# Kernel optimization log

Hardware: AMD Instinct MI355X
Metric: run time of the kernel (lower is better)

The kernel has to match this reference:

```python
import jax, jax.numpy as jnp
import numpy as np


def setup_inputs() -> dict:
    key = jax.random.key(0)
    ks = jax.random.split(key, 6)
    B, C, V, L = 64, 32, 512, 13
    C_OUT = 64
    C_CAT = (2 * 3 + 1) * C  # order*support_len + 1 = 7 blocks -> 224
    x = jax.random.normal(ks[0], (B, C, V, L), dtype=jnp.float32)
    support0 = jax.random.uniform(ks[1], (V, V), dtype=jnp.float32)
    support1 = jax.random.uniform(ks[2], (V, V), dtype=jnp.float32)
    support2 = jax.random.uniform(ks[3], (V, V), dtype=jnp.float32)
    W = jax.random.normal(ks[4], (C_OUT, C_CAT), dtype=jnp.float32) * 0.05
    b = jnp.zeros((C_OUT,), dtype=jnp.float32)
    return {"x": x, "support0": support0, "support1": support1,
            "support2": support2, "W": W, "b": b}


def reference(x, support0, support1, support2, W, b):
    # Graph WaveNet GCN, eval mode (dropout is identity at inference).
    # x: [B, C, V, L]; each support a: [V, V].
    outs = [x]
    for a in (support0, support1, support2):
        x1 = jnp.einsum('ncvl,vw->ncwl', x, a)   # order 1 propagation
        outs.append(x1)
        x2 = jnp.einsum('ncvl,vw->ncwl', x1, a)  # order 2 propagation
        outs.append(x2)
    h = jnp.concatenate(outs, axis=1)            # [B, 7*C, V, L]
    # 1x1 Conv2d == per-(v,l) linear over channels
    h = jnp.einsum('ncvl,oc->novl', h, W) + b[None, :, None, None]
    return h
```

## Files before the change

### kernel.cpp

```cpp
#include <hip/hip_runtime.h>


typedef unsigned short u16;
typedef unsigned int   u32;
typedef __bf16 bf16x8 __attribute__((ext_vector_type(8)));
typedef float  f32x4  __attribute__((ext_vector_type(4)));

#define DEVI static __device__ __forceinline__

#define NB   64
#define NC   32
#define NV   512
#define NL   13
#define CO   64
#define CCAT 224
#define SZA   262144L
#define MSZ   (26624L * 512L)

DEVI u16 f2bf(float f) {
  union { float f; u32 u; } v; v.f = f;
  u32 u = v.u;
  return (u16)((u + 0x7fffu + ((u >> 16) & 1u)) >> 16);
}

DEVI void gl2lds16(const void* g, void* l) {
  __builtin_amdgcn_global_load_lds((__attribute__((address_space(1))) void*)g,
                                   (__attribute__((address_space(3))) void*)l, 16, 0, 0);
}

__global__ __launch_bounds__(256) void prep_A(const float* __restrict__ A0,
                                              const float* __restrict__ A1,
                                              const float* __restrict__ A2,
                                              u16* __restrict__ BT,
                                              u16* __restrict__ ABF) {
  const int s = blockIdx.z;
  const float* A = (s == 0) ? A0 : ((s == 1) ? A1 : A2);
  u16* abf = ABF + (long)s * SZA;
  u16* bt  = BT + (long)(2 * s) * SZA;
  __shared__ float t[32][33];
  const int v0 = blockIdx.x * 32, w0 = blockIdx.y * 32;
  const int tid = threadIdx.x;
  for (int i = tid; i < 1024; i += 256) {
    const int r = i >> 5, c = i & 31;
    const float val = A[(long)(v0 + r) * 512 + w0 + c];
    t[r][c] = val;
    abf[(long)(v0 + r) * 512 + w0 + c] = f2bf(val);
  }
  __syncthreads();
  for (int i = tid; i < 1024; i += 256) {
    const int r = i >> 5, c = i & 31;
    bt[(long)(w0 + r) * 512 + v0 + c] = f2bf(t[c][r]);
  }
}

__global__ __launch_bounds__(256) void prep_W(const float* __restrict__ W,
                                              u16* __restrict__ WBF) {
  const int i = blockIdx.x * 256 + threadIdx.x;
  WBF[i] = f2bf(W[i]);
}

__global__ __launch_bounds__(256) void transpose_x(const float* __restrict__ x,
                                                   u16* __restrict__ XT) {
  __shared__ __align__(16) float tile[NV * NL];
  const int bc = blockIdx.x;
  const float4* src4 = (const float4*)(x + (long)bc * (NV * NL));
  float4* t4 = (float4*)tile;
  for (int i = threadIdx.x; i < (NV * NL) / 4; i += 256) t4[i] = src4[i];
  __syncthreads();
  u16* dst = XT + (long)bc * (NL * NV);
  for (int j = threadIdx.x; j < NL * 256; j += 256) {
    const int l = j >> 8, v = (j & 255) * 2;
    const u32 lo = f2bf(tile[v * NL + l]);
    const u32 hi = f2bf(tile[(v + 1) * NL + l]);
    *(u32*)&dst[l * 512 + v] = lo | (hi << 16);
  }
}

__global__ __launch_bounds__(256) void gemm512(const u16* __restrict__ Ag,
                                               const u16* __restrict__ Bg,
                                               u16* __restrict__ Cg,
                                               long aZ, long bZ, long cZ) {
  __shared__ u16 As[128 * 32];
  __shared__ u16 Bs[128 * 32];
  const int p = blockIdx.z;
  const u16* A = Ag + (long)p * aZ;
  const u16* B = Bg + (long)p * bZ;
  u16*       C = Cg + (long)p * cZ;
  const int m0 = blockIdx.y * 128, n0 = blockIdx.x * 128;
  const int tid = threadIdx.x;
  const int lane = tid & 63, wid = tid >> 6;
  const int wm = wid >> 1, wn = wid & 1;
  const int lr = lane & 15, lq = lane >> 4;
  const int srow = lane >> 2, skq = lane & 3;

  f32x4 acc[4][4] = {};

  for (int kt = 0; kt < 16; ++kt) {
    const int k0 = kt * 32;
    __syncthreads();
#pragma unroll
    for (int j = 0; j < 2; ++j) {
      const int rb = wid * 32 + j * 16;
      gl2lds16(A + (long)(m0 + rb + srow) * 512 + (k0 + skq * 8), &As[rb * 32]);
      gl2lds16(B + (long)(n0 + rb + srow) * 512 + (k0 + skq * 8), &Bs[rb * 32]);
    }
    __syncthreads();
    bf16x8 af[4], bv[4];
#pragma unroll
    for (int t = 0; t < 4; ++t) {
      af[t] = *(const bf16x8*)&As[(wm * 64 + t * 16 + lr) * 32 + lq * 8];
      bv[t] = *(const bf16x8*)&Bs[(wn * 64 + t * 16 + lr) * 32 + lq * 8];
    }
#pragma unroll
    for (int i = 0; i < 4; ++i)
#pragma unroll
      for (int j = 0; j < 4; ++j)
        acc[i][j] = __builtin_amdgcn_mfma_f32_16x16x32_bf16(af[i], bv[j], acc[i][j], 0, 0, 0);
  }
#pragma unroll
  for (int i = 0; i < 4; ++i) {
    const int mr = m0 + wm * 64 + i * 16 + lq * 4;
#pragma unroll
    for (int j = 0; j < 4; ++j) {
      const int nc = n0 + wn * 64 + j * 16 + lr;
#pragma unroll
      for (int r = 0; r < 4; ++r)
        C[(long)(mr + r) * 512 + nc] = f2bf(acc[i][j][r]);
    }
  }
}

__global__ __launch_bounds__(256) void gemm_big(const u16* __restrict__ A,
                                                const u16* __restrict__ Bg,
                                                u16* __restrict__ Cg) {
  __shared__ u16 As[128 * 32];
  __shared__ u16 Bs[128 * 32];
  const int p = blockIdx.x >> 2;
  const int n0 = (blockIdx.x & 3) * 128;
  const int m0 = blockIdx.y * 128;
  const u16* B = Bg + (long)p * SZA;
  u16*       C = Cg + (long)p * MSZ;
  const int tid = threadIdx.x;
  const int lane = tid & 63, wid = tid >> 6;
  const int wm = wid >> 1, wn = wid & 1;
  const int lr = lane & 15, lq = lane >> 4;
  const int srow = lane >> 2, skq = lane & 3;

  f32x4 acc[4][4] = {};

  for (int kt = 0; kt < 16; ++kt) {
    const int k0 = kt * 32;
    __syncthreads();
#pragma unroll
    for (int j = 0; j < 2; ++j) {
      const int rb = wid * 32 + j * 16;
      gl2lds16(A + (long)(m0 + rb + srow) * 512 + (k0 + skq * 8), &As[rb * 32]);
      gl2lds16(B + (long)(n0 + rb + srow) * 512 + (k0 + skq * 8), &Bs[rb * 32]);
    }
    __syncthreads();
    bf16x8 af[4], bv[4];
#pragma unroll
    for (int t = 0; t < 4; ++t) {
      af[t] = *(const bf16x8*)&As[(wm * 64 + t * 16 + lr) * 32 + lq * 8];
      bv[t] = *(const bf16x8*)&Bs[(wn * 64 + t * 16 + lr) * 32 + lq * 8];
    }
#pragma unroll
    for (int i = 0; i < 4; ++i)
#pragma unroll
      for (int j = 0; j < 4; ++j)
        acc[i][j] = __builtin_amdgcn_mfma_f32_16x16x32_bf16(af[i], bv[j], acc[i][j], 0, 0, 0);
  }
#pragma unroll
  for (int i = 0; i < 4; ++i) {
    const int mr = m0 + wm * 64 + i * 16 + lq * 4;
#pragma unroll
    for (int j = 0; j < 4; ++j) {
      const int nc = n0 + wn * 64 + j * 16 + lr;
#pragma unroll
      for (int r = 0; r < 4; ++r)
        C[(long)(mr + r) * 512 + nc] = f2bf(acc[i][j][r]);
    }
  }
}

__global__ __launch_bounds__(512) void proj_out(const u16* __restrict__ Yall,
                                                const u16* __restrict__ WBF,
                                                const float* __restrict__ bias,
                                                float* __restrict__ out) {
  __shared__ u16 Hs[512 * 32];
  const int n = blockIdx.y, wch = blockIdx.x;
  const int w_base = wch * 32;
  const int tid = threadIdx.x;
  const int lane = tid & 63, wid = tid >> 6;
  const int og = wid & 3, th = wid >> 2;
  const int lr = lane & 15, lq = lane >> 4;
  const int c = tid >> 4, q = tid & 15;

  f32x4 acc[16] = {};
  float bia[4];
#pragma unroll
  for (int r = 0; r < 4; ++r) bia[r] = bias[og * 16 + lq * 4 + r];

  const int cchunk = c >> 3, cin = c & 7;

  for (int blk = 0; blk < 7; ++blk) {
    const u16* Yrow = Yall + (long)blk * MSZ + ((long)(n * NC + c) * NL) * 512 + w_base;
    __syncthreads();
    for (int i = q; i < 104; i += 16) {
      const int lp = i >> 3, w4 = i & 7;
      const ushort4 d = *(const ushort4*)(Yrow + lp * 512 + w4 * 4);
      const int colc = ((cchunk ^ (w4 & 3)) << 3) | cin;
      const int rbase = (w4 * 4) * 16 + lp;
      Hs[(rbase +  0) * 32 + colc] = d.x;
      Hs[(rbase + 16) * 32 + colc] = d.y;
      Hs[(rbase + 32) * 32 + colc] = d.z;
      Hs[(rbase + 48) * 32 + colc] = d.w;
    }
    __syncthreads();
    const bf16x8 af = *(const bf16x8*)&WBF[(og * 16 + lr) * CCAT + blk * 32 + lq * 8];
#pragma unroll
    for (int tt = 0; tt < 16; ++tt) {
      const int t = th * 16 + tt;
      const bf16x8 bv = *(const bf16x8*)&Hs[(t * 16 + lr) * 32 + ((lq ^ ((t >> 2) & 3)) << 3)];
      acc[tt] = __builtin_amdgcn_mfma_f32_16x16x32_bf16(af, bv, acc[tt], 0, 0, 0);
    }
  }
  if (lr < NL) {
#pragma unroll
    for (int tt = 0; tt < 16; ++tt) {
      const int w = w_base + th * 16 + tt;
      const long base = (((long)n * CO + og * 16 + lq * 4) * 512 + w) * NL + lr;
#pragma unroll
      for (int r = 0; r < 4; ++r)
        out[base + (long)r * (512 * NL)] = acc[tt][r] + bia[r];
    }
  }
}

extern "C" void kernel_launch(void* const* d_in, const int* in_sizes, int n_in,
                              void* d_out, int out_size, void* d_ws, size_t ws_size,
                              hipStream_t stream) {
  const float* x  = (const float*)d_in[0];
  const float* s0 = (const float*)d_in[1];
  const float* s1 = (const float*)d_in[2];
  const float* s2 = (const float*)d_in[3];
  const float* W  = (const float*)d_in[4];
  const float* b  = (const float*)d_in[5];
  float* out = (float*)d_out;

  char* ws = (char*)d_ws;
  u16* XT  = (u16*)(ws);
  u16* Y   = (u16*)(ws + 27262976L);
  u16* BT  = (u16*)(ws + 190840832L);
  u16* ABF = (u16*)(ws + 193986560L);
  u16* WBF = (u16*)(ws + 195559424L);

  prep_A<<<dim3(16, 16, 3), 256, 0, stream>>>(s0, s1, s2, BT, ABF);
  prep_W<<<dim3(56), 256, 0, stream>>>(W, WBF);
  gemm512<<<dim3(4, 4, 3), 256, 0, stream>>>(BT, ABF, BT + SZA,
                                             2L * SZA, 1L * SZA, 2L * SZA);
  transpose_x<<<dim3(NB * NC), 256, 0, stream>>>(x, XT);
  gemm_big<<<dim3(24, 208), 256, 0, stream>>>(XT, BT, Y);
  proj_out<<<dim3(16, NB), 512, 0, stream>>>(XT, WBF, b, out);
}
```

Measured before the change: 352.6 us.

## Fuse graph propagation GEMMs with output projection in one kernel

Replaces the separate big propagation GEMM, which wrote seven bf16 intermediate blocks to global memory, and the projection kernel that read them back, with a single fused kernel. Each 128x128 tile computes both support-power products, stores the result transposed in LDS and accumulates the 1x1 conv projection directly, so the large intermediate Y buffer and its global round trip disappear. X is relaid as (b,l,c) rows so each tile's rows cover whole channel groups. The fused kernel also double-buffers its LDS staging, swizzles LDS columns and maps blocks to XCDs. In exchange it uses more LDS and registers per block, which may lower occupancy.

```diff
diff --git a/kernel.cpp b/kernel.cpp
--- a/kernel.cpp
+++ b/kernel.cpp
@@ -5,17 +5,16 @@
 typedef unsigned int   u32;
 typedef __bf16 bf16x8 __attribute__((ext_vector_type(8)));
 typedef float  f32x4  __attribute__((ext_vector_type(4)));
+typedef u16    u16x4  __attribute__((ext_vector_type(4)));
+typedef u16    u16x8  __attribute__((ext_vector_type(8)));
 
 #define DEVI static __device__ __forceinline__
 
-#define NB   64
-#define NC   32
 #define NV   512
 #define NL   13
-#define CO   64
-#define CCAT 224
-#define SZA   262144L
-#define MSZ   (26624L * 512L)
+#define SZA  262144L
+#define YP   136
+#define WP   232
 
 DEVI u16 f2bf(float f) {
   union { float f; u32 u; } v; v.f = f;
@@ -63,16 +62,17 @@
                                                    u16* __restrict__ XT) {
   __shared__ __align__(16) float tile[NV * NL];
   const int bc = blockIdx.x;
+  const int b = bc >> 5, c = bc & 31;
   const float4* src4 = (const float4*)(x + (long)bc * (NV * NL));
   float4* t4 = (float4*)tile;
   for (int i = threadIdx.x; i < (NV * NL) / 4; i += 256) t4[i] = src4[i];
   __syncthreads();
-  u16* dst = XT + (long)bc * (NL * NV);
   for (int j = threadIdx.x; j < NL * 256; j += 256) {
     const int l = j >> 8, v = (j & 255) * 2;
+    const long row = (long)(b * 13 + l) * 32 + c;
     const u32 lo = f2bf(tile[v * NL + l]);
     const u32 hi = f2bf(tile[(v + 1) * NL + l]);
-    *(u32*)&dst[l * 512 + v] = lo | (hi << 16);
+    *(u32*)&XT[row * 512 + v] = lo | (hi << 16);
   }
 }
 
@@ -80,8 +80,8 @@
                                                const u16* __restrict__ Bg,
                                                u16* __restrict__ Cg,
                                                long aZ, long bZ, long cZ) {
-  __shared__ u16 As[128 * 32];
-  __shared__ u16 Bs[128 * 32];
+  __shared__ __align__(16) u16 As[128 * 32];
+  __shared__ __align__(16) u16 Bs[128 * 32];
   const int p = blockIdx.z;
   const u16* A = Ag + (long)p * aZ;
   const u16* B = Bg + (long)p * bZ;
@@ -130,111 +130,142 @@
   }
 }
 
-__global__ __launch_bounds__(256) void gemm_big(const u16* __restrict__ A,
-                                                const u16* __restrict__ Bg,
-                                                u16* __restrict__ Cg) {
-  __shared__ u16 As[128 * 32];
-  __shared__ u16 Bs[128 * 32];
-  const int p = blockIdx.x >> 2;
-  const int n0 = (blockIdx.x & 3) * 128;
-  const int m0 = blockIdx.y * 128;
-  const u16* B = Bg + (long)p * SZA;
-  u16*       C = Cg + (long)p * MSZ;
-  const int tid = threadIdx.x;
+__global__ __launch_bounds__(512) void fused_gcn(const u16* __restrict__ XT,
+                                                 const u16* __restrict__ BT,
+                                                 const u16* __restrict__ WBF,
+                                                 const float* __restrict__ bias,
+                                                 float* __restrict__ out) {
+  __shared__ __align__(16) u16 As[2][128 * 32];
+  __shared__ __align__(16) u16 Bs0[2][128 * 32];
+  __shared__ __align__(16) u16 Bs1[2][128 * 32];
+  __shared__ __align__(16) u16 Yt[128 * YP];
+  __shared__ __align__(16) u16 Ws[64 * WP];
+
+  const int P = blockIdx.x;
+  const int xcd = P & 7, inner = P >> 3;
+  const int ym = xcd * 26 + (inner >> 2);
+  const int m0 = ym * 128;
+  const int w0 = (inner & 3) * 128;
+
+  const int tid  = threadIdx.x;
   const int lane = tid & 63, wid = tid >> 6;
-  const int wm = wid >> 1, wn = wid & 1;
   const int lr = lane & 15, lq = lane >> 4;
-  const int srow = lane >> 2, skq = lane & 3;
-
-  f32x4 acc[4][4] = {};
-
-  for (int kt = 0; kt < 16; ++kt) {
-    const int k0 = kt * 32;
-    __syncthreads();
-#pragma unroll
-    for (int j = 0; j < 2; ++j) {
-      const int rb = wid * 32 + j * 16;
-      gl2lds16(A + (long)(m0 + rb + srow) * 512 + (k0 + skq * 8), &As[rb * 32]);
-      gl2lds16(B + (long)(n0 + rb + srow) * 512 + (k0 + skq * 8), &Bs[rb * 32]);
-    }
-    __syncthreads();
-    bf16x8 af[4], bv[4];
-#pragma unroll
-    for (int t = 0; t < 4; ++t) {
-      af[t] = *(const bf16x8*)&As[(wm * 64 + t * 16 + lr) * 32 + lq * 8];
-      bv[t] = *(const bf16x8*)&Bs[(wn * 64 + t * 16 + lr) * 32 + lq * 8];
-    }
-#pragma unroll
-    for (int i = 0; i < 4; ++i)
-#pragma unroll
-      for (int j = 0; j < 4; ++j)
-        acc[i][j] = __builtin_amdgcn_mfma_f32_16x16x32_bf16(af[i], bv[j], acc[i][j], 0, 0, 0);
-  }
-#pragma unroll
-  for (int i = 0; i < 4; ++i) {
-    const int mr = m0 + wm * 64 + i * 16 + lq * 4;
-#pragma unroll
-    for (int j = 0; j < 4; ++j) {
-      const int nc = n0 + wn * 64 + j * 16 + lr;
+  const int wv = wid & 1, wm = wid >> 1;
+  const int g  = wid >> 1, h  = wid & 1;
+  const int srow = tid >> 2, skq = tid & 3;
+  const int scol = (skq ^ ((srow >> 1) & 3)) * 8;
+  const int ldsb = wid * 512;
+  const int co = (lq ^ ((lr >> 1) & 3)) * 8;
+
+  for (int i = tid; i < 64 * 56; i += 512) {
+    const int row = i / 56, c4 = (i - row * 56) * 4;
+    *(u16x4*)&Ws[row * WP + c4] = *(const u16x4*)&WBF[row * 224 + c4];
+  }
+  for (int i = tid; i < 2048; i += 512) {
+    const int mrow = i >> 4, c8 = (i & 15) * 8;
+    const u16x8 d = *(const u16x8*)&XT[(long)(m0 + mrow) * 512 + w0 + c8];
+#pragma unroll
+    for (int z = 0; z < 8; ++z) {
+      const int w = c8 + z;
+      Yt[w * YP + ((((mrow >> 3) ^ ((w >> 3) & 3)) << 3) | (mrow & 7))] = d[z];
+    }
+  }
+  __syncthreads();
+
+  f32x4 oacc[4][4] = {};
+
+#define STAGE(Bp0_, Bp1_, kk, bb) do {                                         \
+    const int kc_ = (kk) * 32 + scol;                                          \
+    gl2lds16(XT     + (long)(m0 + srow) * 512 + kc_, &As [bb][ldsb]);          \
+    gl2lds16((Bp0_) + (long)(w0 + srow) * 512 + kc_, &Bs0[bb][ldsb]);          \
+    gl2lds16((Bp1_) + (long)(w0 + srow) * 512 + kc_, &Bs1[bb][ldsb]);          \
+  } while (0)
+
+#define PROJ(blk) do {                                                         \
+    bf16x8 paf_[4], pbv_[4];                                                   \
+    _Pragma("unroll")                                                          \
+    for (int oi = 0; oi < 4; ++oi)                                             \
+      paf_[oi] = *(const bf16x8*)&Ws[(oi * 16 + lr) * WP + (blk) * 32 + lq * 8]; \
+    _Pragma("unroll")                                                          \
+    for (int wj = 0; wj < 4; ++wj) {                                           \
+      const int w_ = h * 64 + wj * 16 + lr;                                    \
+      pbv_[wj] = *(const bf16x8*)&Yt[w_ * YP + (((g * 4 + lq) ^ ((w_ >> 3) & 3)) << 3)]; \
+    }                                                                          \
+    _Pragma("unroll")                                                          \
+    for (int oi = 0; oi < 4; ++oi)                                             \
+      _Pragma("unroll")                                                        \
+      for (int wj = 0; wj < 4; ++wj)                                           \
+        oacc[oi][wj] = __builtin_amdgcn_mfma_f32_16x16x32_bf16(paf_[oi], pbv_[wj], oacc[oi][wj], 0, 0, 0); \
+  } while (0)
+
+#define WRB(ac) do {                                                           \
+    _Pragma("unroll")                                                          \
+    for (int i = 0; i < 4; ++i)                                                \
+      _Pragma("unroll")                                                        \
+      for (int j = 0; j < 2; ++j)                                              \
+        _Pragma("unroll")                                                      \
+        for (int r = 0; r < 4; ++r) {                                          \
+          const int w_ = wv * 64 + i * 16 + lq * 4 + r;                        \
+          const int m_ = wm * 32 + j * 16 + lr;                                \
+          Yt[w_ * YP + ((((m_ >> 3) ^ ((w_ >> 3) & 3)) << 3) | (m_ & 7))] = f2bf(ac[i][j][r]); \
+        }                                                                      \
+  } while (0)
+
+  for (int pass = 0; pass < 3; ++pass) {
+    const u16* Bp0 = BT + (long)(2 * pass) * SZA;
+    const u16* Bp1 = BT + (long)(2 * pass + 1) * SZA;
+    STAGE(Bp0, Bp1, 0, 0);
+    PROJ(2 * pass);
+    __syncthreads();
+    f32x4 accA[4][2] = {}, accB[4][2] = {};
+    for (int kt = 0; kt < 16; ++kt) {
+      const int buf = kt & 1;
+      if (kt < 15) STAGE(Bp0, Bp1, kt + 1, buf ^ 1);
+      bf16x8 a0[4], a1[4], bv[2];
+#pragma unroll
+      for (int i = 0; i < 4; ++i) {
+        a0[i] = *(const bf16x8*)&Bs0[buf][(wv * 64 + i * 16 + lr) * 32 + co];
+        a1[i] = *(const bf16x8*)&Bs1[buf][(wv * 64 + i * 16 + lr) * 32 + co];
+      }
+#pragma unroll
+      for (int j = 0; j < 2; ++j)
+        bv[j] = *(const bf16x8*)&As[buf][(wm * 32 + j * 16 + lr) * 32 + co];
+#pragma unroll
+      for (int i = 0; i < 4; ++i)
+#pragma unroll
+        for (int j = 0; j < 2; ++j) {
+          accA[i][j] = __builtin_amdgcn_mfma_f32_16x16x32_bf16(a0[i], bv[j], accA[i][j], 0, 0, 0);
+          accB[i][j] = __builtin_amdgcn_mfma_f32_16x16x32_bf16(a1[i], bv[j], accB[i][j], 0, 0, 0);
+        }
+      __syncthreads();
+    }
+    WRB(accA);
+    __syncthreads();
+    PROJ(2 * pass + 1);
+    __syncthreads();
+    WRB(accB);
+    __syncthreads();
+  }
+  PROJ(6);
+
+  const int bl = ym * 4 + g;
+  const int b  = bl / 13, l = bl - b * 13;
+  float* outb = out + (long)b * (64L * 512 * 13) + l;
+#pragma unroll
+  for (int oi = 0; oi < 4; ++oi) {
+    const f32x4 bi = *(const f32x4*)&bias[oi * 16 + lq * 4];
+#pragma unroll
+    for (int wj = 0; wj < 4; ++wj) {
+      const int w = w0 + h * 64 + wj * 16 + lr;
+      const long base = ((long)(oi * 16 + lq * 4) * 512 + w) * 13;
 #pragma unroll
       for (int r = 0; r < 4; ++r)
-        C[(long)(mr + r) * 512 + nc] = f2bf(acc[i][j][r]);
-    }
-  }
-}
-
-__global__ __launch_bounds__(512) void proj_out(const u16* __restrict__ Yall,
-                                                const u16* __restrict__ WBF,
-                                                const float* __restrict__ bias,
-                                                float* __restrict__ out) {
-  __shared__ u16 Hs[512 * 32];
-  const int n = blockIdx.y, wch = blockIdx.x;
-  const int w_base = wch * 32;
-  const int tid = threadIdx.x;
-  const int lane = tid & 63, wid = tid >> 6;
-  const int og = wid & 3, th = wid >> 2;
-  const int lr = lane & 15, lq = lane >> 4;
-  const int c = tid >> 4, q = tid & 15;
-
-  f32x4 acc[16] = {};
-  float bia[4];
-#pragma unroll
-  for (int r = 0; r < 4; ++r) bia[r] = bias[og * 16 + lq * 4 + r];
-
-  const int cchunk = c >> 3, cin = c & 7;
-
-  for (int blk = 0; blk < 7; ++blk) {
-    const u16* Yrow = Yall + (long)blk * MSZ + ((long)(n * NC + c) * NL) * 512 + w_base;
-    __syncthreads();
-    for (int i = q; i < 104; i += 16) {
-      const int lp = i >> 3, w4 = i & 7;
-      const ushort4 d = *(const ushort4*)(Yrow + lp * 512 + w4 * 4);
-      const int colc = ((cchunk ^ (w4 & 3)) << 3) | cin;
-      const int rbase = (w4 * 4) * 16 + lp;
-      Hs[(rbase +  0) * 32 + colc] = d.x;
-      Hs[(rbase + 16) * 32 + colc] = d.y;
-      Hs[(rbase + 32) * 32 + colc] = d.z;
-      Hs[(rbase + 48) * 32 + colc] = d.w;
-    }
-    __syncthreads();
-    const bf16x8 af = *(const bf16x8*)&WBF[(og * 16 + lr) * CCAT + blk * 32 + lq * 8];
-#pragma unroll
-    for (int tt = 0; tt < 16; ++tt) {
-      const int t = th * 16 + tt;
-      const bf16x8 bv = *(const bf16x8*)&Hs[(t * 16 + lr) * 32 + ((lq ^ ((t >> 2) & 3)) << 3)];
-      acc[tt] = __builtin_amdgcn_mfma_f32_16x16x32_bf16(af, bv, acc[tt], 0, 0, 0);
-    }
-  }
-  if (lr < NL) {
-#pragma unroll
-    for (int tt = 0; tt < 16; ++tt) {
-      const int w = w_base + th * 16 + tt;
-      const long base = (((long)n * CO + og * 16 + lq * 4) * 512 + w) * NL + lr;
-#pragma unroll
-      for (int r = 0; r < 4; ++r)
-        out[base + (long)r * (512 * NL)] = acc[tt][r] + bia[r];
-    }
-  }
+        outb[base + (long)r * (512 * 13)] = oacc[oi][wj][r] + bi[r];
+    }
+  }
+#undef STAGE
+#undef PROJ
+#undef WRB
 }
 
 extern "C" void kernel_launch(void* const* d_in, const int* in_sizes, int n_in,
@@ -250,16 +281,14 @@
 
   char* ws = (char*)d_ws;
   u16* XT  = (u16*)(ws);
-  u16* Y   = (u16*)(ws + 27262976L);
-  u16* BT  = (u16*)(ws + 190840832L);
-  u16* ABF = (u16*)(ws + 193986560L);
-  u16* WBF = (u16*)(ws + 195559424L);
+  u16* BT  = (u16*)(ws + 27262976L);
+  u16* ABF = (u16*)(ws + 30408704L);
+  u16* WBF = (u16*)(ws + 31981568L);
 
   prep_A<<<dim3(16, 16, 3), 256, 0, stream>>>(s0, s1, s2, BT, ABF);
   prep_W<<<dim3(56), 256, 0, stream>>>(W, WBF);
   gemm512<<<dim3(4, 4, 3), 256, 0, stream>>>(BT, ABF, BT + SZA,
                                              2L * SZA, 1L * SZA, 2L * SZA);
-  transpose_x<<<dim3(NB * NC), 256, 0, stream>>>(x, XT);
-  gemm_big<<<dim3(24, 208), 256, 0, stream>>>(XT, BT, Y);
-  proj_out<<<dim3(16, NB), 512, 0, stream>>>(XT, WBF, b, out);
-}
+  transpose_x<<<dim3(64 * 32), 256, 0, stream>>>(x, XT);
+  fused_gcn<<<dim3(832), 512, 0, stream>>>(XT, BT, WBF, b, out);
+}
```

New measurement: 446.2 us. +26.5%, slower.
